# Performance work log

Measured on AMD Instinct MI355X. Metric: run time of the kernel, lower is better.

Reference implementation:

```python
import jax, jax.numpy as jnp
import numpy as np

B, N, E = 8, 10000, 320000   # graphs, nodes per graph, edges per graph
C_IN, C_OUT = 128, 128


def setup_inputs() -> dict:
    key = jax.random.key(0)
    k_x, k_w, k_b, k_r, k_c, k_n = jax.random.split(key, 6)
    x = jax.random.normal(k_x, (B, N, C_IN), dtype=jnp.float32)
    weight = jax.random.normal(k_w, (C_IN, C_OUT), dtype=jnp.float32)
    bias = jax.random.normal(k_b, (C_OUT,), dtype=jnp.float32)
    edge_row = jax.random.randint(k_r, (B, E), 0, N, dtype=jnp.int32)
    edge_col = jax.random.randint(k_c, (B, E), 0, N, dtype=jnp.int32)
    edge_val = jnp.ones((B, E), dtype=jnp.float32)
    num_nodes = jax.random.randint(k_n, (B,), 1, N, dtype=jnp.int32)
    return {"x": x, "weight": weight, "bias": bias,
            "edge_row": edge_row, "edge_col": edge_col, "edge_val": edge_val,
            "num_nodes": num_nodes}


def reference(x, weight, bias, edge_row, edge_col, edge_val, num_nodes):
    # x: [B, N, C_in] -> linear transform
    h = jnp.einsum('bnc,co->bno', x, weight) + bias          # [B, N, C_out]

    def spmm_one(rows, cols, vals, h_b):
        # A @ h_b for one graph via gather + segment-sum scatter
        msgs = vals[:, None] * h_b[cols]                      # [E, C_out]
        agg = jax.ops.segment_sum(msgs, rows, num_segments=N) # [N, C_out]
        deg = jax.ops.segment_sum(vals, rows, num_segments=N) # row sums of A
        return agg / jnp.clip(deg, 1.0)[:, None]              # clamp(min=1)

    out = jax.vmap(spmm_one)(edge_row, edge_col, edge_val, h)  # [B, N, C_out]

    # zero out padded nodes: out[i, num_nodes[i]:, :] = 0
    mask = jnp.arange(N)[None, :] < num_nodes[:, None]         # [B, N]
    return out * mask[:, :, None].astype(out.dtype)
```

## Files before the change

### kernel.cpp

```cpp
#include <hip/hip_runtime.h>

#define BG   8
#define NN   10000
#define EE   320000
#define CC   128
#define BN   (BG*NN)
#define BE   (BG*EE)

#define NBKT   157
#define BROWS  64
#define CAP    2560
#define CHUNK  4096
#define BPG    ((EE + CHUNK - 1) / CHUNK)


__global__ __launch_bounds__(256) void k_bin(const int* __restrict__ edge_row,
                                             const int* __restrict__ edge_col,
                                             const float* __restrict__ edge_val,
                                             int* __restrict__ cursor,
                                             int2* __restrict__ binned) {
    int g = blockIdx.x / BPG;
    int cstart = (blockIdx.x % BPG) * CHUNK;
    int t = threadIdx.x;
    __shared__ int lh[NBKT];
    __shared__ int lbase[NBKT];
    for (int i = t; i < NBKT; i += 256) lh[i] = 0;
    __syncthreads();
    int rows[CHUNK / 256];
    int pos[CHUNK / 256];
#pragma unroll
    for (int j = 0; j < CHUNK / 256; j++) {
        int e = cstart + j * 256 + t;
        if (e < EE) {
            int r = edge_row[(size_t)g * EE + e];
            rows[j] = r;
            pos[j] = atomicAdd(&lh[r >> 6], 1);
        } else rows[j] = -1;
    }
    __syncthreads();
    for (int i = t; i < NBKT; i += 256) {
        int c = lh[i];
        lbase[i] = c ? atomicAdd(&cursor[g * NBKT + i], c) : 0;
    }
    __syncthreads();
#pragma unroll
    for (int j = 0; j < CHUNK / 256; j++) {
        if (rows[j] >= 0) {
            int e = cstart + j * 256 + t;
            int r = rows[j];
            int bkt = r >> 6;
            binned[((size_t)g * NBKT + bkt) * CAP + lbase[bkt] + pos[j]] =
                make_int2(((r & 63) << 14) | edge_col[(size_t)g * EE + e],
                          __float_as_int(edge_val[(size_t)g * EE + e]));
        }
    }
}

__global__ __launch_bounds__(256) void k_sort(const int2* __restrict__ binned,
                                              const int* __restrict__ bcnt,
                                              int2* __restrict__ sorted,
                                              int* __restrict__ row_off,
                                              int* __restrict__ row_cnt,
                                              float* __restrict__ deg) {
    int g = blockIdx.x / NBKT;
    int bkt = blockIdx.x % NBKT;
    int t = threadIdx.x;
    __shared__ int2 ein[CAP];
    __shared__ int2 eout[CAP];
    __shared__ int cnts[BROWS], excl[BROWS], curs[BROWS];
    __shared__ float degl[BROWS];
    if (t < BROWS) { cnts[t] = 0; degl[t] = 0.f; }
    __syncthreads();
    int cnt = bcnt[g * NBKT + bkt];
    if (cnt > CAP) cnt = CAP;
    const int2* src = binned + ((size_t)g * NBKT + bkt) * CAP;
    for (int i = t; i < cnt; i += 256) {
        int2 ed = src[i];
        ein[i] = ed;
        atomicAdd(&cnts[ed.x >> 14], 1);
        atomicAdd(&degl[ed.x >> 14], __int_as_float(ed.y));
    }
    __syncthreads();
    if (t < 64) {
        int own = cnts[t];
        int v = own;
#pragma unroll
        for (int d = 1; d < 64; d <<= 1) {
            int n = __shfl_up(v, d);
            if (t >= d) v += n;
        }
        excl[t] = v - own;
        curs[t] = v - own;
        int gr = bkt * BROWS + t;
        if (gr < NN) {
            int row = g * NN + gr;
            row_off[row] = bkt * CAP + (v - own);
            row_cnt[row] = own;
            deg[row] = degl[t];
        }
    }
    __syncthreads();
    for (int i = t; i < cnt; i += 256) {
        int2 ed = ein[i];
        int pos = atomicAdd(&curs[ed.x >> 14], 1);
        eout[pos] = make_int2(ed.x & 0x3FFF, ed.y);
    }
    __syncthreads();
    int2* dst = sorted + ((size_t)g * NBKT + bkt) * CAP;
    for (int i = t; i < cnt; i += 256) dst[i] = eout[i];
}

__global__ __launch_bounds__(256) void k_gather(const float* __restrict__ x,
                                                const int* __restrict__ row_off,
                                                const int* __restrict__ row_cnt,
                                                const int2* __restrict__ sorted,
                                                float* __restrict__ aggx,
                                                int pass) {
    int bid = blockIdx.x;
    int g = bid & 7;
    int chunk = bid >> 3;
    int wid = threadIdx.x >> 6, lane = threadIdx.x & 63;
    int r = chunk * 4 + wid;
    int bn = g * NN + r;
    int start = __builtin_amdgcn_readfirstlane(row_off[bn]);
    int cnt = __builtin_amdgcn_readfirstlane(row_cnt[bn]);
    const float* xb = x + (size_t)g * NN * CC + pass * 64 + lane;
    const long long* ep =
        (const long long*)(sorted + (size_t)g * NBKT * CAP + start);

    float a0 = 0.f, a1 = 0.f;
    int e = 0;
    for (; e + 8 <= cnt; e += 8) {
        int c[8]; float v[8];
#pragma unroll
        for (int j = 0; j < 8; j++) {
            long long m = __builtin_nontemporal_load(ep + e + j);
            c[j] = __builtin_amdgcn_readfirstlane((int)m);
            v[j] = __int_as_float(__builtin_amdgcn_readfirstlane((int)(m >> 32)));
        }
        float xv[8];
#pragma unroll
        for (int j = 0; j < 8; j++)
            xv[j] = xb[(size_t)c[j] << 7];
#pragma unroll
        for (int j = 0; j < 8; j++) {
            if (j & 1) a1 += v[j] * xv[j];
            else       a0 += v[j] * xv[j];
        }
    }
    for (; e < cnt; e++) {
        long long m = __builtin_nontemporal_load(ep + e);
        int c0 = __builtin_amdgcn_readfirstlane((int)m);
        float v0 = __int_as_float(__builtin_amdgcn_readfirstlane((int)(m >> 32)));
        a0 += v0 * xb[(size_t)c0 << 7];
    }
    aggx[(size_t)bn * CC + pass * 64 + lane] = a0 + a1;
}

__global__ __launch_bounds__(256) void k_gemm(float* __restrict__ io,
                                              const float* __restrict__ W,
                                              const float* __restrict__ bias,
                                              const float* __restrict__ deg,
                                              const int* __restrict__ num_nodes) {
    __shared__ float4 wl[64 * 32];
    int t = threadIdx.x;
    const float4* Wv = (const float4*)W;

    int row0 = blockIdx.x * 64;
    int cg = t & 15;
    int rg = t >> 4;
    const float* ap = io + (size_t)(row0 + rg * 4) * CC;

    float acc[4][8] = {};
    for (int h = 0; h < 2; h++) {
        __syncthreads();
#pragma unroll
        for (int i = 0; i < 8; i++)
            wl[t + i * 256] = Wv[h * 2048 + t + i * 256];
        __syncthreads();
        int kbase = h * 64;
        for (int kc = 0; kc < 64; kc += 4) {
            float4 a[4];
#pragma unroll
            for (int i = 0; i < 4; i++)
                a[i] = *(const float4*)(ap + (size_t)i * CC + kbase + kc);
#pragma unroll
            for (int kk = 0; kk < 4; kk++) {
                float4 w0 = wl[(kc + kk) * 32 + cg];
                float4 w1 = wl[(kc + kk) * 32 + 16 + cg];
#pragma unroll
                for (int i = 0; i < 4; i++) {
                    float av = (kk == 0) ? a[i].x : (kk == 1) ? a[i].y
                             : (kk == 2) ? a[i].z : a[i].w;
                    acc[i][0] += av * w0.x; acc[i][1] += av * w0.y;
                    acc[i][2] += av * w0.z; acc[i][3] += av * w0.w;
                    acc[i][4] += av * w1.x; acc[i][5] += av * w1.y;
                    acc[i][6] += av * w1.z; acc[i][7] += av * w1.w;
                }
            }
        }
    }

    float4 b0 = *(const float4*)(bias + cg * 4);
    float4 b1 = *(const float4*)(bias + 64 + cg * 4);
    float bb[8] = { b0.x, b0.y, b0.z, b0.w, b1.x, b1.y, b1.z, b1.w };

#pragma unroll
    for (int i = 0; i < 4; i++) {
        int grow = row0 + rg * 4 + i;
        int b = grow / NN;
        int r = grow - b * NN;
        float d = deg[grow];
        float sc = 1.0f / fmaxf(d, 1.0f);
        bool alive = r < num_nodes[b];
        float o[8];
#pragma unroll
        for (int j = 0; j < 8; j++)
            o[j] = alive ? (acc[i][j] + d * bb[j]) * sc : 0.0f;
        float* dst = io + (size_t)grow * CC;
        *(float4*)(dst + cg * 4)      = make_float4(o[0], o[1], o[2], o[3]);
        *(float4*)(dst + 64 + cg * 4) = make_float4(o[4], o[5], o[6], o[7]);
    }
}

extern "C" void kernel_launch(void* const* d_in, const int* in_sizes, int n_in,
                              void* d_out, int out_size, void* d_ws, size_t ws_size,
                              hipStream_t stream) {
    const float* x        = (const float*)d_in[0];
    const float* weight   = (const float*)d_in[1];
    const float* bias     = (const float*)d_in[2];
    const int*   edge_row = (const int*)d_in[3];
    const int*   edge_col = (const int*)d_in[4];
    const float* edge_val = (const float*)d_in[5];
    const int*   num_nodes= (const int*)d_in[6];
    float* out = (float*)d_out;

    int2*  binned  = (int2*)d_out;
    int2*  sorted  = (int2*)d_ws;
    float* deg     = (float*)(sorted + (size_t)BG * NBKT * CAP);
    int*   row_off = (int*)(deg + BN);
    int*   row_cnt = row_off + BN;
    int*   cursor  = row_cnt + BN;

    hipMemsetAsync(cursor, 0, BG * NBKT * sizeof(int), stream);
    k_bin<<<BG * BPG, 256, 0, stream>>>(edge_row, edge_col, edge_val, cursor, binned);
    k_sort<<<BG * NBKT, 256, 0, stream>>>(binned, cursor, sorted,
                                          row_off, row_cnt, deg);
    k_gather<<<8 * (NN / 4), 256, 0, stream>>>(x, row_off, row_cnt, sorted, out, 0);
    k_gather<<<8 * (NN / 4), 256, 0, stream>>>(x, row_off, row_cnt, sorted, out, 1);
    k_gemm<<<BN / 64, 256, 0, stream>>>(out, weight, bias, deg, num_nodes);
}
```

Baseline: 293.1 us.

## Software-pipeline the edge gather loop with double-buffered prefetch

Restructures the per-row gather loop in k_gather into a two-stage software pipeline. The next groups of packed (col,val) edge records and their x rows are loaded while the current group is accumulated, to hide global-memory latency. It also drops the nontemporal loads and merges the two accumulators into one. The cost is more live registers, which may lower occupancy, and the prefetch reads edge records past a row's count.

```diff
diff --git a/kernel.cpp b/kernel.cpp
--- a/kernel.cpp
+++ b/kernel.cpp
@@ -12,6 +12,8 @@
 #define CAP    2560
 #define CHUNK  4096
 #define BPG    ((EE + CHUNK - 1) / CHUNK)
+
+#define RFL(x) __builtin_amdgcn_readfirstlane(x)
 
 
 __global__ __launch_bounds__(256) void k_bin(const int* __restrict__ edge_row,
@@ -122,39 +124,84 @@
     int wid = threadIdx.x >> 6, lane = threadIdx.x & 63;
     int r = chunk * 4 + wid;
     int bn = g * NN + r;
-    int start = __builtin_amdgcn_readfirstlane(row_off[bn]);
-    int cnt = __builtin_amdgcn_readfirstlane(row_cnt[bn]);
+    int start = RFL(row_off[bn]);
+    int cnt = RFL(row_cnt[bn]);
     const float* xb = x + (size_t)g * NN * CC + pass * 64 + lane;
     const long long* ep =
         (const long long*)(sorted + (size_t)g * NBKT * CAP + start);
 
-    float a0 = 0.f, a1 = 0.f;
+    float acc = 0.f;
+    int G = cnt >> 3;
     int e = 0;
-    for (; e + 8 <= cnt; e += 8) {
-        int c[8]; float v[8];
+    if (G >= 2) {
+        long long rawE[8], rawO[8];
+        float xvE[8], xvO[8];
+        float vE[8], vO[8];
+#pragma unroll
+        for (int j = 0; j < 8; j++) rawE[j] = ep[j];
+#pragma unroll
+        for (int j = 0; j < 8; j++) rawO[j] = ep[8 + j];
+        int cE[8], cO[8];
 #pragma unroll
         for (int j = 0; j < 8; j++) {
-            long long m = __builtin_nontemporal_load(ep + e + j);
-            c[j] = __builtin_amdgcn_readfirstlane((int)m);
-            v[j] = __int_as_float(__builtin_amdgcn_readfirstlane((int)(m >> 32)));
-        }
-        float xv[8];
-#pragma unroll
-        for (int j = 0; j < 8; j++)
-            xv[j] = xb[(size_t)c[j] << 7];
-#pragma unroll
-        for (int j = 0; j < 8; j++) {
-            if (j & 1) a1 += v[j] * xv[j];
-            else       a0 += v[j] * xv[j];
-        }
+            cE[j] = RFL((int)rawE[j]);
+            vE[j] = __int_as_float(RFL((int)(rawE[j] >> 32)));
+        }
+#pragma unroll
+        for (int j = 0; j < 8; j++) xvE[j] = xb[(size_t)cE[j] << 7];
+#pragma unroll
+        for (int j = 0; j < 8; j++) rawE[j] = ep[16 + j];
+
+        int gi = 1;
+        for (; gi + 1 < G; gi += 2) {
+#pragma unroll
+            for (int j = 0; j < 8; j++) {
+                cO[j] = RFL((int)rawO[j]);
+                vO[j] = __int_as_float(RFL((int)(rawO[j] >> 32)));
+            }
+#pragma unroll
+            for (int j = 0; j < 8; j++) xvO[j] = xb[(size_t)cO[j] << 7];
+#pragma unroll
+            for (int j = 0; j < 8; j++) rawO[j] = ep[(gi + 2) * 8 + j];
+#pragma unroll
+            for (int j = 0; j < 8; j++) acc += vE[j] * xvE[j];
+#pragma unroll
+            for (int j = 0; j < 8; j++) {
+                cE[j] = RFL((int)rawE[j]);
+                vE[j] = __int_as_float(RFL((int)(rawE[j] >> 32)));
+            }
+#pragma unroll
+            for (int j = 0; j < 8; j++) xvE[j] = xb[(size_t)cE[j] << 7];
+#pragma unroll
+            for (int j = 0; j < 8; j++) rawE[j] = ep[(gi + 3) * 8 + j];
+#pragma unroll
+            for (int j = 0; j < 8; j++) acc += vO[j] * xvO[j];
+        }
+        if (gi < G) {
+#pragma unroll
+            for (int j = 0; j < 8; j++) {
+                cO[j] = RFL((int)rawO[j]);
+                vO[j] = __int_as_float(RFL((int)(rawO[j] >> 32)));
+            }
+#pragma unroll
+            for (int j = 0; j < 8; j++) xvO[j] = xb[(size_t)cO[j] << 7];
+#pragma unroll
+            for (int j = 0; j < 8; j++) acc += vE[j] * xvE[j];
+#pragma unroll
+            for (int j = 0; j < 8; j++) acc += vO[j] * xvO[j];
+        } else {
+#pragma unroll
+            for (int j = 0; j < 8; j++) acc += vE[j] * xvE[j];
+        }
+        e = G * 8;
     }
     for (; e < cnt; e++) {
-        long long m = __builtin_nontemporal_load(ep + e);
-        int c0 = __builtin_amdgcn_readfirstlane((int)m);
-        float v0 = __int_as_float(__builtin_amdgcn_readfirstlane((int)(m >> 32)));
-        a0 += v0 * xb[(size_t)c0 << 7];
-    }
-    aggx[(size_t)bn * CC + pass * 64 + lane] = a0 + a1;
+        long long m = ep[e];
+        int c0 = RFL((int)m);
+        float v0 = __int_as_float(RFL((int)(m >> 32)));
+        acc += v0 * xb[(size_t)c0 << 7];
+    }
+    aggx[(size_t)bn * CC + pass * 64 + lane] = acc;
 }
 
 __global__ __launch_bounds__(256) void k_gemm(float* __restrict__ io,
```

New measurement: 285.8 us. -2.5%, faster.
